# Kernel optimization log

Hardware: AMD Instinct MI355X
Metric: run time of the kernel (lower is better)

The kernel has to match this reference:

```python
import jax, jax.numpy as jnp
import numpy as np

MAX_VISIT = 200
NUM_CODE = 506          # feature vocab -> 507 multi-hot dims
NUM_TGT = 284           # target vocab multi-hot dims
B = 64
P = 40                  # codes per visit
D_OTH = 57              # others feature dim (sign slice [37:] is 20-dim)
K = 100                 # len(weight_idx)
LSTM = 256
D_FEAT = (NUM_CODE + 1) + K + 27 + (D_OTH - 37)   # 654
D_FWD = D_FEAT + 10                                # 664
D_MLP_IN = (NUM_CODE + 1) + (D_OTH - 37) + 20 + 8  # 555


def multi_hot(codes, n):
    """Binary multi-hot encode int codes over last axis. codes: [..., P]."""
    shp = codes.shape
    flat = codes.reshape(-1, shp[-1])
    R = flat.shape[0]
    rows = jnp.repeat(jnp.arange(R), shp[-1])
    z = jnp.zeros((R, n), jnp.float32).at[rows, flat.reshape(-1)].set(1.0)
    return z.reshape(shp[:-1] + (n,))


def reverse_sequence(x, lengths):
    """tf.reverse_sequence along axis 1: reverse first lengths[i] steps, keep rest."""
    T = x.shape[1]
    j = jnp.arange(T)[None, :]
    L = lengths[:, None]
    idx = jnp.where(j < L, L - 1 - j, j)          # [B, T]
    return jnp.take_along_axis(x, idx[:, :, None], axis=1)


def setup_inputs() -> dict:
    key = jax.random.key(0)
    ks = jax.random.split(key, 13)
    code = jax.random.randint(ks[0], (B, MAX_VISIT, P), 0, NUM_CODE + 1, dtype=jnp.int32)
    others = jax.random.normal(ks[1], (B, MAX_VISIT, D_OTH), jnp.float32)
    length = jax.random.randint(ks[2], (B,), 3, MAX_VISIT + 1, dtype=jnp.int32)
    target = jax.random.randint(ks[3], (B, 10), 0, NUM_TGT, dtype=jnp.int32)
    weight_idx = jax.random.randint(ks[4], (K,), 0, NUM_TGT, dtype=jnp.int32)
    s = 0.02
    Wf = jax.random.normal(ks[5], (D_FWD, LSTM), jnp.float32) * s
    bf = jnp.zeros((LSTM,), jnp.float32)
    Wb = jax.random.normal(ks[6], (D_FWD, LSTM), jnp.float32) * s
    bb = jnp.zeros((LSTM,), jnp.float32)
    W0 = jax.random.normal(ks[7], (D_MLP_IN, 256), jnp.float32) * s
    b0 = jnp.zeros((256,), jnp.float32)
    W1 = jax.random.normal(ks[8], (256, 256), jnp.float32) * s
    b1 = jnp.zeros((256,), jnp.float32)
    return {"code": code, "others": others, "length": length, "target": target,
            "weight_idx": weight_idx, "Wf": Wf, "bf": bf, "Wb": Wb, "bb": bb,
            "W0": W0, "b0": b0, "W1": W1, "b1": b1}


def reference(code, others, length, target, weight_idx, Wf, bf, Wb, bb, W0, b0, W1, b1):
    code_mh = multi_hot(code, NUM_CODE + 1)                      # [B,200,507]
    # valid-visit mask (dense analogue of tf.boolean_mask over [B,198])
    mask = (jnp.arange(MAX_VISIT - 2)[None, :] < (length - 2)[:, None]).astype(jnp.float32)
    sign = others[:, 1:-1, 37:]                                  # [B,198,20]
    interval_ = jnp.concatenate([others[:, 1:-1, 27:37], others[:, 2:, 27:37]], axis=-1)
    stay = others[:, 1:-1, 19:27]
    x = jnp.concatenate([code_mh[:, 1:-1], sign, interval_, stay], axis=-1)  # [B,198,555]
    h = jax.nn.relu(x @ W0 + b0) @ W1 + b1                       # [B,198,256]
    fv = h / jnp.sqrt(jnp.sum(h * h, axis=-1, keepdims=True))
    fv = fv * mask[:, :, None]                                   # zero invalid rows
    # target block: gather (1 - multi-hot) at weight_idx, tile over visits
    tgt = 1.0 - multi_hot(target, NUM_TGT)                       # [B,284]
    tgt = tgt[:, weight_idx]                                     # [B,K]
    tgt = jnp.broadcast_to(tgt[:, None, :], (B, MAX_VISIT, K))
    code_full = jnp.concatenate([code_mh, tgt], axis=-1)         # [B,200,607]
    interval = others[:, :, 27:37]
    interval_backward = jnp.concatenate(
        [jnp.zeros((B, 1, 10), jnp.float32), reverse_sequence(interval, length)[:, :-1]], axis=1)
    feature = jnp.concatenate([code_full, others[:, :, :27], others[:, :, 37:]], axis=-1)
    feature_backward = reverse_sequence(feature, length)
    x_forward = jnp.concatenate([feature, interval], axis=-1)[:, :-2] @ Wf + bf
    x_backward = jnp.concatenate([feature_backward, interval_backward], axis=-1)[:, :-2] @ Wb + bb
    return (x_forward, x_backward, fv)
```

## Files before the change

### kernel.cpp

```cpp
#include <hip/hip_runtime.h>
#include <hip/hip_bf16.h>

typedef unsigned short u16;
typedef __attribute__((ext_vector_type(8))) short short8;
typedef __attribute__((ext_vector_type(4))) float f32x4;

#define TMAX 200
#define TOUT 198
#define PC 40
#define DOTH 57
#define NKT 9
#define FWD_OFF 0
#define BWD_OFF 3244032
#define FV_OFF  6488064
#define OWF 0
#define OWB 294912
#define OW0 589824
#define OW1 884736
#define OTF 1015808
#define OTB 1081344

__device__ __forceinline__ u16 f2b(float v) {
  __hip_bfloat16 h = __float2bfloat16(v);
  return *(u16*)&h;
}

__global__ __launch_bounds__(256) void prep_kernel(
    const int* __restrict__ target, const int* __restrict__ widx,
    const float* __restrict__ Wf, const float* __restrict__ bfv,
    const float* __restrict__ Wb, const float* __restrict__ bbv,
    const float* __restrict__ W0, const float* __restrict__ W1,
    u16* __restrict__ wsu, float* __restrict__ wsf)
{
  int blk = blockIdx.x, n = threadIdx.x;
  if (blk < 248) {
    const float* src; u16* dst; int kb; int mode;
    if (blk < 72)       { src=Wf; dst=wsu+OWF/2; kb=blk;     mode=0; }
    else if (blk < 144) { src=Wb; dst=wsu+OWB/2; kb=blk-72;  mode=0; }
    else if (blk < 216) { src=W0; dst=wsu+OW0/2; kb=blk-144; mode=1; }
    else                { src=W1; dst=wsu+OW1/2; kb=blk-216; mode=2; }
    u16 pk[8];
    #pragma unroll
    for (int j=0;j<8;j++) {
      int k = kb*8+j;
      int sr;
      if (mode==0)      sr = (k<57)? 607+k : (k<564)? k-57 : -1;
      else if (mode==1) sr = (k<48)? 507+k : (k<57)? -1 : (k<564)? k-57 : -1;
      else              sr = k;
      float v = (sr>=0)? src[sr*256+n] : 0.f;
      pk[j] = f2b(v);
    }
    *(uint4*)(dst + (kb*256+n)*8) = *(uint4*)pk;
  } else {
    int b = blk - 248;
    __shared__ float tval[100]; __shared__ int tg[10];
    if (n<10) tg[n]=target[b*10+n];
    __syncthreads();
    if (n<100){ int w=widx[n]; float v=1.f;
      #pragma unroll
      for(int i=0;i<10;i++) if(tg[i]==w) v=0.f;
      tval[n]=v; }
    __syncthreads();
    float aF=bfv[n], aB=bbv[n];
    for(int k=0;k<100;k++){ float v=tval[k];
      aF=fmaf(v,Wf[(507+k)*256+n],aF); aB=fmaf(v,Wb[(507+k)*256+n],aB); }
    wsf[OTF/4 + b*256+n]=aF; wsf[OTB/4 + b*256+n]=aB;
  }
}

__global__ __launch_bounds__(256) void gemm_kernel(
    const int* __restrict__ code, const float* __restrict__ others,
    const int* __restrict__ length,
    const float* __restrict__ b0, const float* __restrict__ b1,
    const u16* __restrict__ wsu, const float* __restrict__ wsf,
    float* __restrict__ out)
{
  const int tile = blockIdx.x;
  const int strm = blockIdx.y;
  const int tid = threadIdx.x;
  const int wv = tid>>6, lane = tid&63, q = lane>>4, c = lane&15;
  const int colbase = wv*64 + c;

  __shared__ u16 lA[3][2048];
  __shared__ int rowB[32], rowT[32], rowS[32], rowS2[32], rowL[32];
  __shared__ float rpart[4][32];
  __shared__ int s_skip;

  if (tid == 0) s_skip = 1;
  if (tid < 32) {
    int m = tile*32 + tid;
    int b = m/198, t = m - b*198;
    int L = length[b];
    int s, s2 = 0;
    if (strm==0) s = t;
    else if (strm==1){ s = (t<L)? (L-1-t) : t;
                       s2 = (t==0)? -1 : (((t-1)<L)? (L-t) : (t-1)); }
    else s = t+1;
    rowB[tid]=b; rowT[tid]=t; rowS[tid]=s; rowS2[tid]=s2; rowL[tid]=L;
  }
  __syncthreads();

  if (strm == 2) {
    if (tid < 32 && rowT[tid] < rowL[tid]-2) s_skip = 0;
    __syncthreads();
    if (s_skip) {
      f32x4 z = {0.f, 0.f, 0.f, 0.f};
      #pragma unroll
      for (int it=0; it<8; it++) {
        int lin = it*256 + tid;
        int r = lin>>6, c4 = (lin&63)<<2;
        *(f32x4*)(out + FV_OFF + (rowB[r]*TOUT + rowT[r])*256 + c4) = z;
      }
      return;
    }
  }

  int myp[5], myr[5];
  #pragma unroll
  for (int it=0; it<5; it++) {
    int idx = tid + it*256;
    int r = idx/40, p = idx - r*40;
    myr[it] = r*8;
    myp[it] = 57 + code[(rowB[r]*TMAX + rowS[r])*PC + p];
  }

  float dv[8];
  if (strm < 2) {
    #pragma unroll
    for (int it=0; it<8; it++) {
      int idx = tid + it*256;
      float v = 0.f;
      if (idx < 32*57) {
        int r = idx/57, j = idx - r*57;
        int col = (j<27)? j : (j<47)? 37+(j-27) : 27+(j-47);
        int sr = (strm==1 && j>=47)? rowS2[r] : rowS[r];
        if (sr >= 0) v = others[(rowB[r]*TMAX + sr)*DOTH + col];
      }
      dv[it] = v;
    }
  } else {
    #pragma unroll
    for (int it=0; it<6; it++) {
      int idx = tid + it*256;
      int r = idx/48, j = idx - r*48;
      int t = rowT[r], srow, col;
      if (j<20)      { srow=t+1; col=37+j; }
      else if (j<30) { srow=t+1; col=27+(j-20); }
      else if (j<40) { srow=t+2; col=27+(j-30); }
      else           { srow=t+1; col=19+(j-40); }
      dv[it] = others[(rowB[r]*TMAX + srow)*DOTH + col];
    }
  }

  f32x4 acc[2][4];
  if (strm < 2) {
    const float* tg = wsf + ((strm==0)? OTF/4 : OTB/4);
    #pragma unroll
    for (int mt=0; mt<2; mt++)
      #pragma unroll
      for (int reg=0; reg<4; reg++) {
        int rl = mt*16 + q*4 + reg;
        const float* tr = tg + rowB[rl]*256;
        #pragma unroll
        for (int nt=0; nt<4; nt++) acc[mt][nt][reg] = tr[colbase + nt*16];
      }
  } else {
    #pragma unroll
    for (int nt=0; nt<4; nt++){ float v = b0[colbase + nt*16];
      #pragma unroll
      for (int mt=0; mt<2; mt++)
        #pragma unroll
        for (int reg=0; reg<4; reg++) acc[mt][nt][reg]=v; }
  }

  const u16* Wpk = wsu + ((strm==0)? OWF/2 : (strm==1)? OWB/2 : OW0/2);
  short8 bb[2][8];
  {
    const u16* gB0 = Wpk + ((q    )*256 + colbase)*8;
    const u16* gB1 = Wpk + ((4 + q)*256 + colbase)*8;
    #pragma unroll
    for (int nt=0; nt<4; nt++) {
      bb[0][nt]   = *(const short8*)(gB0 + nt*128);
      bb[0][nt+4] = *(const short8*)(gB1 + nt*128);
    }
  }

  { uint4 z = {0,0,0,0};
    ((uint4*)lA[0])[tid] = z; ((uint4*)lA[1])[tid] = z; }
  __syncthreads();
  #pragma unroll
  for (int it=0; it<5; it++) {
    unsigned d = (unsigned)(myp[it]);
    if (d < 64u) lA[0][(d>>3)*256 + myr[it] + (d&7)] = 0x3F80;
  }
  if (strm < 2) {
    #pragma unroll
    for (int it=0; it<8; it++) {
      int idx = tid + it*256;
      if (idx < 32*57) {
        int r = idx/57, j = idx - r*57;
        lA[0][(j>>3)*256 + r*8 + (j&7)] = f2b(dv[it]);
      }
    }
  } else {
    #pragma unroll
    for (int it=0; it<6; it++) {
      int idx = tid + it*256;
      int r = idx/48, j = idx - r*48;
      lA[0][(j>>3)*256 + r*8 + (j&7)] = f2b(dv[it]);
    }
  }
  __syncthreads();

  #pragma unroll
  for (int kt=0; kt<NKT; kt++) {
    const u16* A = lA[kt%3];
    short8 af0[2], af1[2];
    #pragma unroll
    for (int mt=0; mt<2; mt++) af0[mt] = *(const short8*)&A[(q    )*256 + (mt*16 + c)*8];
    #pragma unroll
    for (int mt=0; mt<2; mt++) af1[mt] = *(const short8*)&A[(4 + q)*256 + (mt*16 + c)*8];
    if (kt < NKT-1) {
      const u16* gB0 = Wpk + (((kt+1)*8 + q    )*256 + colbase)*8;
      const u16* gB1 = Wpk + (((kt+1)*8 + 4 + q)*256 + colbase)*8;
      #pragma unroll
      for (int nt=0; nt<4; nt++) {
        bb[(kt+1)&1][nt]   = *(const short8*)(gB0 + nt*128);
        bb[(kt+1)&1][nt+4] = *(const short8*)(gB1 + nt*128);
      }
    }
    if (kt < NKT-1) {
      u16* nb = lA[(kt+1)%3];
      const int k0n = (kt+1)*64;
      #pragma unroll
      for (int it=0; it<5; it++) {
        unsigned d = (unsigned)(myp[it] - k0n);
        if (d < 64u) nb[(d>>3)*256 + myr[it] + (d&7)] = 0x3F80;
      }
    }
    if (kt < NKT-2) {
      uint4 z = {0,0,0,0};
      ((uint4*)lA[(kt+2)%3])[tid] = z;
    }
    #pragma unroll
    for (int mt=0; mt<2; mt++)
      #pragma unroll
      for (int nt=0; nt<4; nt++)
        acc[mt][nt] = __builtin_amdgcn_mfma_f32_16x16x32_bf16(af0[mt], bb[kt&1][nt], acc[mt][nt], 0,0,0);
    #pragma unroll
    for (int mt=0; mt<2; mt++)
      #pragma unroll
      for (int nt=0; nt<4; nt++)
        acc[mt][nt] = __builtin_amdgcn_mfma_f32_16x16x32_bf16(af1[mt], bb[kt&1][nt+4], acc[mt][nt], 0,0,0);
    __syncthreads();
  }

  if (strm < 2) {
    float* o = out + ((strm==0)? FWD_OFF : BWD_OFF);
    #pragma unroll
    for (int mt=0; mt<2; mt++)
      #pragma unroll
      for (int reg=0; reg<4; reg++) {
        int rl = mt*16 + q*4 + reg;
        float* orow = o + (rowB[rl]*TOUT + rowT[rl])*256 + colbase;
        #pragma unroll
        for (int nt=0; nt<4; nt++) orow[nt*16] = acc[mt][nt][reg];
      }
  } else {
    if (wv == 0) {
      #pragma unroll
      for (int mt=0; mt<2; mt++)
        #pragma unroll
        for (int reg=0; reg<4; reg++) {
          int rl = mt*16 + q*4 + reg;
          #pragma unroll
          for (int nt=0; nt<4; nt++) {
            int kl = c + nt*16;
            lA[0][(kl>>3)*256 + rl*8 + (kl&7)] = f2b(fmaxf(acc[mt][nt][reg], 0.f));
          }
        }
    }
    const u16* W1p = wsu + OW1/2;
    short8 bw[2][4];
    {
      const u16* gB = W1p + ((q)*256 + colbase)*8;
      #pragma unroll
      for (int nt=0; nt<4; nt++) bw[0][nt] = *(const short8*)(gB + nt*128);
    }
    __syncthreads();
    f32x4 a2[2][4];
    #pragma unroll
    for (int nt=0; nt<4; nt++){ float v = b1[colbase + nt*16];
      #pragma unroll
      for (int mt=0; mt<2; mt++)
        #pragma unroll
        for (int reg=0; reg<4; reg++) a2[mt][nt][reg]=v; }
    #pragma unroll
    for (int kt2=0; kt2<4; kt2++) {
      if (wv == kt2+1) {
        u16* B2 = lA[(kt2+1)&1];
        #pragma unroll
        for (int mt=0; mt<2; mt++)
          #pragma unroll
          for (int reg=0; reg<4; reg++) {
            int rl = mt*16 + q*4 + reg;
            #pragma unroll
            for (int nt=0; nt<4; nt++) {
              int kl = c + nt*16;
              B2[(kl>>3)*256 + rl*8 + (kl&7)] = f2b(fmaxf(acc[mt][nt][reg], 0.f));
            }
          }
      }
      #pragma unroll
      for (int s=0; s<2; s++) {
        const int step = kt2*2 + s;
        const u16* A2 = lA[kt2&1];
        int akb = s*4 + q;
        short8 af[2];
        #pragma unroll
        for (int mt=0; mt<2; mt++) af[mt] = *(const short8*)&A2[akb*256 + (mt*16 + c)*8];
        if (step < 7) {
          const int nstep = step + 1;
          const u16* gB = W1p + (((nstep>>1)*8 + (nstep&1)*4 + q)*256 + colbase)*8;
          #pragma unroll
          for (int nt=0; nt<4; nt++) bw[nstep&1][nt] = *(const short8*)(gB + nt*128);
        }
        #pragma unroll
        for (int mt=0; mt<2; mt++)
          #pragma unroll
          for (int nt=0; nt<4; nt++)
            a2[mt][nt] = __builtin_amdgcn_mfma_f32_16x16x32_bf16(af[mt], bw[step&1][nt], a2[mt][nt], 0,0,0);
      }
      __syncthreads();
    }
    #pragma unroll
    for (int mt=0; mt<2; mt++)
      #pragma unroll
      for (int reg=0; reg<4; reg++) {
        int rl = mt*16 + q*4 + reg;
        float ss = 0.f;
        #pragma unroll
        for (int nt=0; nt<4; nt++){ float v=a2[mt][nt][reg]; ss = fmaf(v,v,ss); }
        ss += __shfl_xor(ss, 1, 64); ss += __shfl_xor(ss, 2, 64);
        ss += __shfl_xor(ss, 4, 64); ss += __shfl_xor(ss, 8, 64);
        if (c==0) rpart[wv][rl] = ss;
      }
    __syncthreads();
    #pragma unroll
    for (int mt=0; mt<2; mt++)
      #pragma unroll
      for (int reg=0; reg<4; reg++) {
        int rl = mt*16 + q*4 + reg;
        float s = rpart[0][rl]+rpart[1][rl]+rpart[2][rl]+rpart[3][rl];
        float inv = (s>0.f)? (1.0f/sqrtf(s)) : 0.f;
        int t = rowT[rl];
        if (t >= rowL[rl]-2) inv = 0.f;
        float* orow = out + FV_OFF + (rowB[rl]*TOUT + t)*256 + colbase;
        #pragma unroll
        for (int nt=0; nt<4; nt++) orow[nt*16] = a2[mt][nt][reg]*inv;
      }
  }
}

extern "C" void kernel_launch(void* const* d_in, const int* in_sizes, int n_in,
                              void* d_out, int out_size, void* d_ws, size_t ws_size,
                              hipStream_t stream) {
  const int*   code    = (const int*)d_in[0];
  const float* others  = (const float*)d_in[1];
  const int*   length  = (const int*)d_in[2];
  const int*   target  = (const int*)d_in[3];
  const int*   widx    = (const int*)d_in[4];
  const float* Wf      = (const float*)d_in[5];
  const float* bfv     = (const float*)d_in[6];
  const float* Wb      = (const float*)d_in[7];
  const float* bbv     = (const float*)d_in[8];
  const float* W0      = (const float*)d_in[9];
  const float* b0v     = (const float*)d_in[10];
  const float* W1      = (const float*)d_in[11];
  const float* b1v     = (const float*)d_in[12];

  u16*   wsu = (u16*)d_ws;
  float* wsf = (float*)d_ws;
  float* out = (float*)d_out;

  prep_kernel<<<dim3(312), dim3(256), 0, stream>>>(target, widx, Wf, bfv, Wb, bbv, W0, W1, wsu, wsf);
  gemm_kernel<<<dim3(396,3), dim3(256), 0, stream>>>(code, others, length,
      b0v, b1v, wsu, wsf, out);
}
```

Before: 121.4 us.

## Stage whole A tile in LDS upfront and move workspace to a device global

The A operand (multi-hot codes plus dense features) for all nine K-steps is now built in shared memory before the MFMA loop, which removes the per-step zeroing, scatter and __syncthreads from the main loop. Shared memory per block grows from three 4 KB buffers to nine (about 36 KB), which may reduce how many blocks fit on a CU. The workspace also moves from the harness-provided buffer to a static __device__ array. That array is shared between calls and would race if launches overlap.

```diff
diff --git a/kernel.cpp b/kernel.cpp
--- a/kernel.cpp
+++ b/kernel.cpp
@@ -19,6 +19,9 @@
 #define OW1 884736
 #define OTF 1015808
 #define OTB 1081344
+#define WS_BYTES 1146880
+
+__device__ __align__(16) unsigned char g_ws[WS_BYTES];
 
 __device__ __forceinline__ u16 f2b(float v) {
   __hip_bfloat16 h = __float2bfloat16(v);
@@ -29,9 +32,10 @@
     const int* __restrict__ target, const int* __restrict__ widx,
     const float* __restrict__ Wf, const float* __restrict__ bfv,
     const float* __restrict__ Wb, const float* __restrict__ bbv,
-    const float* __restrict__ W0, const float* __restrict__ W1,
-    u16* __restrict__ wsu, float* __restrict__ wsf)
+    const float* __restrict__ W0, const float* __restrict__ W1)
 {
+  u16*   wsu = (u16*)g_ws;
+  float* wsf = (float*)g_ws;
   int blk = blockIdx.x, n = threadIdx.x;
   if (blk < 248) {
     const float* src; u16* dst; int kb; int mode;
@@ -72,16 +76,17 @@
     const int* __restrict__ code, const float* __restrict__ others,
     const int* __restrict__ length,
     const float* __restrict__ b0, const float* __restrict__ b1,
-    const u16* __restrict__ wsu, const float* __restrict__ wsf,
     float* __restrict__ out)
 {
+  const u16*   wsu = (const u16*)g_ws;
+  const float* wsf = (const float*)g_ws;
   const int tile = blockIdx.x;
   const int strm = blockIdx.y;
   const int tid = threadIdx.x;
   const int wv = tid>>6, lane = tid&63, q = lane>>4, c = lane&15;
   const int colbase = wv*64 + c;
 
-  __shared__ u16 lA[3][2048];
+  __shared__ u16 lA[NKT*2048];
   __shared__ int rowB[32], rowT[32], rowS[32], rowS2[32], rowL[32];
   __shared__ float rpart[4][32];
   __shared__ int s_skip;
@@ -186,12 +191,14 @@
   }
 
   { uint4 z = {0,0,0,0};
-    ((uint4*)lA[0])[tid] = z; ((uint4*)lA[1])[tid] = z; }
+    #pragma unroll
+    for (int i=0; i<NKT; i++) ((uint4*)lA)[tid + i*256] = z;
+  }
   __syncthreads();
   #pragma unroll
   for (int it=0; it<5; it++) {
-    unsigned d = (unsigned)(myp[it]);
-    if (d < 64u) lA[0][(d>>3)*256 + myr[it] + (d&7)] = 0x3F80;
+    int d = myp[it];
+    lA[(d>>3)*256 + myr[it] + (d&7)] = 0x3F80;
   }
   if (strm < 2) {
     #pragma unroll
@@ -199,7 +206,7 @@
       int idx = tid + it*256;
       if (idx < 32*57) {
         int r = idx/57, j = idx - r*57;
-        lA[0][(j>>3)*256 + r*8 + (j&7)] = f2b(dv[it]);
+        lA[(j>>3)*256 + r*8 + (j&7)] = f2b(dv[it]);
       }
     }
   } else {
@@ -207,14 +214,14 @@
     for (int it=0; it<6; it++) {
       int idx = tid + it*256;
       int r = idx/48, j = idx - r*48;
-      lA[0][(j>>3)*256 + r*8 + (j&7)] = f2b(dv[it]);
+      lA[(j>>3)*256 + r*8 + (j&7)] = f2b(dv[it]);
     }
   }
   __syncthreads();
 
   #pragma unroll
   for (int kt=0; kt<NKT; kt++) {
-    const u16* A = lA[kt%3];
+    const u16* A = lA + kt*2048;
     short8 af0[2], af1[2];
     #pragma unroll
     for (int mt=0; mt<2; mt++) af0[mt] = *(const short8*)&A[(q    )*256 + (mt*16 + c)*8];
@@ -229,19 +236,6 @@
         bb[(kt+1)&1][nt+4] = *(const short8*)(gB1 + nt*128);
       }
     }
-    if (kt < NKT-1) {
-      u16* nb = lA[(kt+1)%3];
-      const int k0n = (kt+1)*64;
-      #pragma unroll
-      for (int it=0; it<5; it++) {
-        unsigned d = (unsigned)(myp[it] - k0n);
-        if (d < 64u) nb[(d>>3)*256 + myr[it] + (d&7)] = 0x3F80;
-      }
-    }
-    if (kt < NKT-2) {
-      uint4 z = {0,0,0,0};
-      ((uint4*)lA[(kt+2)%3])[tid] = z;
-    }
     #pragma unroll
     for (int mt=0; mt<2; mt++)
       #pragma unroll
@@ -252,7 +246,6 @@
       #pragma unroll
       for (int nt=0; nt<4; nt++)
         acc[mt][nt] = __builtin_amdgcn_mfma_f32_16x16x32_bf16(af1[mt], bb[kt&1][nt+4], acc[mt][nt], 0,0,0);
-    __syncthreads();
   }
 
   if (strm < 2) {
@@ -267,6 +260,7 @@
         for (int nt=0; nt<4; nt++) orow[nt*16] = acc[mt][nt][reg];
       }
   } else {
+    __syncthreads();
     if (wv == 0) {
       #pragma unroll
       for (int mt=0; mt<2; mt++)
@@ -276,7 +270,7 @@
           #pragma unroll
           for (int nt=0; nt<4; nt++) {
             int kl = c + nt*16;
-            lA[0][(kl>>3)*256 + rl*8 + (kl&7)] = f2b(fmaxf(acc[mt][nt][reg], 0.f));
+            lA[(kl>>3)*256 + rl*8 + (kl&7)] = f2b(fmaxf(acc[mt][nt][reg], 0.f));
           }
         }
     }
@@ -298,7 +292,7 @@
     #pragma unroll
     for (int kt2=0; kt2<4; kt2++) {
       if (wv == kt2+1) {
-        u16* B2 = lA[(kt2+1)&1];
+        u16* B2 = lA + ((kt2+1)&1)*2048;
         #pragma unroll
         for (int mt=0; mt<2; mt++)
           #pragma unroll
@@ -314,7 +308,7 @@
       #pragma unroll
       for (int s=0; s<2; s++) {
         const int step = kt2*2 + s;
-        const u16* A2 = lA[kt2&1];
+        const u16* A2 = lA + (kt2&1)*2048;
         int akb = s*4 + q;
         short8 af[2];
         #pragma unroll
@@ -378,12 +372,10 @@
   const float* b0v     = (const float*)d_in[10];
   const float* W1      = (const float*)d_in[11];
   const float* b1v     = (const float*)d_in[12];
-
-  u16*   wsu = (u16*)d_ws;
-  float* wsf = (float*)d_ws;
+  (void)d_ws; (void)ws_size;
+
   float* out = (float*)d_out;
 
-  prep_kernel<<<dim3(312), dim3(256), 0, stream>>>(target, widx, Wf, bfv, Wb, bbv, W0, W1, wsu, wsf);
-  gemm_kernel<<<dim3(396,3), dim3(256), 0, stream>>>(code, others, length,
-      b0v, b1v, wsu, wsf, out);
+  prep_kernel<<<dim3(312), dim3(256), 0, stream>>>(target, widx, Wf, bfv, Wb, bbv, W0, W1);
+  gemm_kernel<<<dim3(396,3), dim3(256), 0, stream>>>(code, others, length, b0v, b1v, out);
 }
```

Result: slower. 124.6 us (+2.7%).
